# Kernel optimization log

Measured on AMD Instinct MI355X. Metric: run time of the kernel, lower is better.

## Reference

```python
import jax, jax.numpy as jnp
import numpy as np

N = 2048
HID = 1024
Z = 256
DIM = 128 + 64 * 3 + 32 * 5  # 480
FAN = 128 * 128 + 64 * 64 + 32 * 32  # total fan-in over all CG paths


def _ln(x, g, b, eps=1e-6):
    mu = jnp.mean(x, axis=-1, keepdims=True)
    var = jnp.mean((x - mu) ** 2, axis=-1, keepdims=True)
    return (x - mu) * jax.lax.rsqrt(var + eps) * g + b


def _fctp(t, w0, w1, w2):
    # FullyConnectedTensorProduct(irreps, irreps, 'HIDx0e'):
    # only l1==l2 -> 0e paths survive; CG is delta_{m1,m2}/sqrt(2l+1).
    x0 = t[:, :128]                       # 128x0e
    x1 = t[:, 128:320].reshape(-1, 64, 3)  # 64x1o
    x2 = t[:, 320:480].reshape(-1, 32, 5)  # 32x2e
    e0 = jnp.einsum('bu,bv,uvh->bh', x0, x0, w0)
    e1 = jnp.einsum('bum,bvm,uvh->bh', x1, x1, w1) / np.sqrt(3.0)
    e2 = jnp.einsum('bum,bvm,uvh->bh', x2, x2, w2) / np.sqrt(5.0)
    return (e0 + e1 + e2) / np.sqrt(float(FAN))  # component normalization


def _head(t, w0, w1, w2, W1, b1, g1, be1, W2, b2, g2, be2):
    h = _fctp(t, w0, w1, w2)
    h = jax.nn.silu(_ln(h @ W1 + b1, g1, be1))
    h = jax.nn.silu(_ln(h @ W2 + b2, g2, be2))
    return h  # [N, Z]


def setup_inputs() -> dict:
    key = jax.random.key(0)
    ks = jax.random.split(key, 6)
    return {
        'tensor_in': jax.random.normal(ks[0], (N, DIM), jnp.float32),
        'w0': jax.random.normal(ks[1], (128, 128, HID), jnp.float32),
        'w1': jax.random.normal(ks[2], (64, 64, HID), jnp.float32),
        'w2': jax.random.normal(ks[3], (32, 32, HID), jnp.float32),
        'W1': jax.random.normal(ks[4], (HID, HID), jnp.float32) / np.sqrt(HID),
        'b1': jnp.zeros((HID,), jnp.float32),
        'g1': jnp.ones((HID,), jnp.float32),
        'be1': jnp.zeros((HID,), jnp.float32),
        'W2': jax.random.normal(ks[5], (HID, Z), jnp.float32) / np.sqrt(HID),
        'b2': jnp.zeros((Z,), jnp.float32),
        'g2': jnp.ones((Z,), jnp.float32),
        'be2': jnp.zeros((Z,), jnp.float32),
    }


def reference(tensor_in, w0, w1, w2, W1, b1, g1, be1, W2, b2, g2, be2):
    f = lambda t: _head(t, w0, w1, w2, W1, b1, g1, be1, W2, b2, g2, be2)
    x, pullback = jax.vjp(f, tensor_in)
    # torch: grad(x, tensor_in, grad_outputs=ones_like(x), create_graph=True)
    y = pullback(jnp.ones_like(x))[0]
    return x, y
```

## Files before the change

kernel.cpp:

```cpp
#include <hip/hip_runtime.h>
#include <math.h>

typedef unsigned short u16;
typedef __bf16 bf16x8 __attribute__((ext_vector_type(8)));
typedef float f32x4 __attribute__((ext_vector_type(4)));

#define NPACK  11264
#define NVALID 10864
#define BASE1  8256
#define BASE2  10336

__device__ __forceinline__ u16 f2bf(float f) {
    unsigned u = __builtin_bit_cast(unsigned, f);
    u += 0x7FFFu + ((u >> 16) & 1u);
    return (u16)(u >> 16);
}
__device__ __forceinline__ float bf2f(u16 h) {
    return __builtin_bit_cast(float, ((unsigned)h) << 16);
}

#define GLOAD_LDS16(g, l)                                                     \
    __builtin_amdgcn_global_load_lds(                                         \
        (const __attribute__((address_space(1))) void*)(g),                   \
        (__attribute__((address_space(3))) void*)(l), 16, 0, 0)

__device__ __forceinline__ int pk0(int a, int b) {
    int u = min(a, b), v = max(a, b);
    return u * 128 - (u * (u - 1)) / 2 + (v - u);
}
__device__ __forceinline__ int pk1(int a, int b) {
    int u = min(a, b), v = max(a, b);
    return BASE1 + u * 64 - (u * (u - 1)) / 2 + (v - u);
}
__device__ __forceinline__ int pk2(int a, int b) {
    int u = min(a, b), v = max(a, b);
    return BASE2 + u * 32 - (u * (u - 1)) / 2 + (v - u);
}

__device__ __forceinline__ void prep_transpose(const float* __restrict__ in, int C,
                                               u16* __restrict__ out, int ldOut,
                                               int bx, int by, int tid) {
    __shared__ float tile[32][33];
    int tr0 = by * 32, tc0 = bx * 32;
    int lr = tid >> 5, lc = tid & 31;
#pragma unroll
    for (int i = 0; i < 4; i++) {
        int rr = lr + i * 8;
        tile[rr][lc] = in[(size_t)(tr0 + rr) * C + tc0 + lc];
    }
    __syncthreads();
#pragma unroll
    for (int i = 0; i < 4; i++) {
        int rr = lr + i * 8;
        out[(size_t)(tc0 + rr) * ldOut + tr0 + lc] = f2bf(tile[lc][rr]);
    }
}
__device__ __forceinline__ void prep_convert(const float* __restrict__ in,
                                             u16* __restrict__ out, int i, int n4) {
    if (i >= n4) return;
    float4 v = ((const float4*)in)[i];
    union { u16 a[4]; unsigned long long q; } o;
    o.a[0] = f2bf(v.x); o.a[1] = f2bf(v.y); o.a[2] = f2bf(v.z); o.a[3] = f2bf(v.w);
    ((unsigned long long*)out)[i] = o.q;
}

__global__ __launch_bounds__(256) void k_prep(u16* __restrict__ tab,
                                              const float* __restrict__ W1,
                                              const float* __restrict__ W2,
                                              u16* __restrict__ W1b,
                                              u16* __restrict__ W1tb,
                                              u16* __restrict__ W2b,
                                              u16* __restrict__ W2tb) {
    int bid = blockIdx.x, tid = threadIdx.x;
    if (bid < 86) {
        int j = bid * 256 + tid;
        if (j < 16384) {
            int u = j >> 7, v = j & 127;
            if (v >= u) tab[pk0(u, v)] = (u16)((u << 7) | v);
        } else if (j < 20480) {
            int k = j - 16384, u = k >> 6, v = k & 63;
            if (v >= u) tab[pk1(u, v)] = (u16)((1 << 14) | (u << 7) | v);
        } else if (j < 21504) {
            int k = j - 20480, u = k >> 5, v = k & 31;
            if (v >= u) tab[pk2(u, v)] = (u16)((2 << 14) | (u << 7) | v);
        } else if (j < 21504 + (NPACK - NVALID)) {
            tab[NVALID + (j - 21504)] = 0xFFFFu;
        }
    } else if (bid < 1110) {
        int k = bid - 86;
        prep_transpose(W1, 1024, W1tb, 1024, k & 31, k >> 5, tid);
    } else if (bid < 1366) {
        int k = bid - 1110;
        prep_transpose(W2, 256, W2tb, 1024, k & 7, k >> 3, tid);
    } else if (bid < 2390) {
        prep_convert(W1, W1b, (bid - 1366) * 256 + tid, 1024 * 1024 / 4);
    } else {
        prep_convert(W2, W2b, (bid - 2390) * 256 + tid, 1024 * 256 / 4);
    }
}

__global__ __launch_bounds__(256) void k_packw(const float* __restrict__ w0,
                                               const float* __restrict__ w1,
                                               const float* __restrict__ w2,
                                               const u16* __restrict__ tab,
                                               u16* __restrict__ Wsym,
                                               u16* __restrict__ Wt) {
    __shared__ u16 tile[32][258];
    __shared__ u16 te[32];
    int i0 = blockIdx.x * 32, h0 = blockIdx.y * 256, tid = threadIdx.x;
    if (tid < 32) te[tid] = tab[i0 + tid];
    __syncthreads();
    const float s1 = 0.57735026918962576f, s2 = 0.44721359549995794f;
    for (int il = 0; il < 32; il++) {
        unsigned e = te[il];
        float val = 0.f;
        if ((e >> 14) != 3) {
            int seg = e >> 14, u = (e >> 7) & 127, v = e & 127;
            const float* wb; int S; float sc;
            if (seg == 0)      { wb = w0; S = 128; sc = 1.f; }
            else if (seg == 1) { wb = w1; S = 64;  sc = s1; }
            else               { wb = w2; S = 32;  sc = s2; }
            val = sc * (wb[(size_t)(u * S + v) * 1024 + h0 + tid] +
                        wb[(size_t)(v * S + u) * 1024 + h0 + tid]);
        }
        u16 bv = f2bf(val);
        Wsym[(size_t)(i0 + il) * 1024 + h0 + tid] = bv;
        tile[il][tid] = bv;
    }
    __syncthreads();
    union { u16 a[32]; uint4 q[4]; } pk;
#pragma unroll
    for (int il = 0; il < 32; il++) pk.a[il] = tile[il][tid];
    uint4* dst = (uint4*)(Wt + (size_t)(h0 + tid) * NPACK + i0);
#pragma unroll
    for (int q = 0; q < 4; q++) dst[q] = pk.q[q];
}

__global__ __launch_bounds__(256) void k_features_pack(const float* __restrict__ t,
                                                       const u16* __restrict__ tab,
                                                       u16* __restrict__ P) {
    __shared__ u16 tab_s[NPACK];
    __shared__ float tr[480];
    int b = blockIdx.x, tid = threadIdx.x;
    for (int j = tid; j < NPACK / 8; j += 256)
        ((uint4*)tab_s)[j] = ((const uint4*)tab)[j];
    for (int j = tid; j < 480; j += 256) tr[j] = t[(size_t)b * 480 + j];
    __syncthreads();
    u16* row = P + (size_t)b * NPACK;
    for (int i = tid; i < NPACK; i += 256) {
        unsigned e = tab_s[i];
        float p = 0.f;
        if ((e >> 14) != 3) {
            int seg = e >> 14, u = (e >> 7) & 127, v = e & 127;
            if (seg == 0) p = tr[u] * tr[v];
            else if (seg == 1) {
                const float* x1 = tr + 128;
                p = x1[u*3]*x1[v*3] + x1[u*3+1]*x1[v*3+1] + x1[u*3+2]*x1[v*3+2];
            } else {
                const float* x2 = tr + 320;
#pragma unroll
                for (int m = 0; m < 5; m++) p += x2[u*5+m] * x2[v*5+m];
            }
            if (u == v) p *= 0.5f;
        }
        row[i] = f2bf(p);
    }
}

__global__ __launch_bounds__(256) void k_gemm2(const u16* __restrict__ A, int ldA,
                                               const u16* __restrict__ B, int ldB,
                                               int kLen, float scale,
                                               const float* __restrict__ bias,
                                               float* __restrict__ Cf,
                                               u16* __restrict__ Cb, int ldC,
                                               u16* __restrict__ Cpart, int Mtot,
                                               int swz) {
    __shared__ u16 As[2][128 * 32];
    __shared__ u16 Bs[2][128 * 32];
    const int tid = threadIdx.x;
    const int wave = tid >> 6, lane = tid & 63;
    const int wm = wave >> 1, wn = wave & 1;
    int nT, mT, z;
    if (swz == 1) {
        int L = blockIdx.x;
        z = L & 7; int r = L >> 3;
        nT = r >> 4; mT = r & 15;
    } else if (swz == 2) {
        int L = blockIdx.x;
        int c = L & 7, r = L >> 3;
        nT = (r % 11) * 8 + c; mT = r / 11; z = 0;
    } else {
        nT = blockIdx.x; mT = blockIdx.y; z = blockIdx.z;
    }
    const int m0 = mT * 128, n0 = nT * 128;
    const size_t kOff = (size_t)z * kLen;

    const int chl = (((lane & 3) ^ ((lane >> 3) & 3))) * 8;
    const u16* aG = A + (size_t)(m0 + wave * 32 + (lane >> 2)) * ldA + kOff + chl;
    const u16* bG = B + (size_t)(n0 + wave * 32 + (lane >> 2)) * ldB + kOff + chl;
    const size_t aS = (size_t)16 * ldA;
    const size_t bS = (size_t)16 * ldB;
    u16* aL0 = &As[0][(wave * 32) * 32];
    u16* aL1 = &As[0][(wave * 32 + 16) * 32];
    u16* aH0 = &As[1][(wave * 32) * 32];
    u16* aH1 = &As[1][(wave * 32 + 16) * 32];
    u16* bL0 = &Bs[0][(wave * 32) * 32];
    u16* bL1 = &Bs[0][(wave * 32 + 16) * 32];
    u16* bH0 = &Bs[1][(wave * 32) * 32];
    u16* bH1 = &Bs[1][(wave * 32 + 16) * 32];

    f32x4 acc[4][4];
#pragma unroll
    for (int i = 0; i < 4; i++)
#pragma unroll
        for (int j = 0; j < 4; j++) acc[i][j] = (f32x4){0.f, 0.f, 0.f, 0.f};

    const int ml = lane & 15, kq8 = lane >> 4;
    const int kqs = (kq8 ^ ((ml >> 1) & 3)) * 8;
    const u16* aRd0 = &As[0][(wm * 64 + ml) * 32 + kqs];
    const u16* bRd0 = &Bs[0][(wn * 64 + ml) * 32 + kqs];
    const u16* aRd1 = &As[1][(wm * 64 + ml) * 32 + kqs];
    const u16* bRd1 = &Bs[1][(wn * 64 + ml) * 32 + kqs];

    for (int k = 0; k < kLen; k += 64) {
        GLOAD_LDS16(aG, aL0);
        GLOAD_LDS16(aG + aS, aL1);
        GLOAD_LDS16(aG + 32, aH0);
        GLOAD_LDS16(aG + aS + 32, aH1);
        GLOAD_LDS16(bG, bL0);
        GLOAD_LDS16(bG + bS, bL1);
        GLOAD_LDS16(bG + 32, bH0);
        GLOAD_LDS16(bG + bS + 32, bH1);
        aG += 64; bG += 64;
        __syncthreads();
        {
            bf16x8 af[4], bfv[4];
#pragma unroll
            for (int i = 0; i < 4; i++) af[i]  = *(const bf16x8*)(aRd0 + i * 16 * 32);
#pragma unroll
            for (int j = 0; j < 4; j++) bfv[j] = *(const bf16x8*)(bRd0 + j * 16 * 32);
#pragma unroll
            for (int i = 0; i < 4; i++)
#pragma unroll
                for (int j = 0; j < 4; j++)
                    acc[i][j] = __builtin_amdgcn_mfma_f32_16x16x32_bf16(af[i], bfv[j], acc[i][j], 0, 0, 0);
        }
        {
            bf16x8 af[4], bfv[4];
#pragma unroll
            for (int i = 0; i < 4; i++) af[i]  = *(const bf16x8*)(aRd1 + i * 16 * 32);
#pragma unroll
            for (int j = 0; j < 4; j++) bfv[j] = *(const bf16x8*)(bRd1 + j * 16 * 32);
#pragma unroll
            for (int i = 0; i < 4; i++)
#pragma unroll
                for (int j = 0; j < 4; j++)
                    acc[i][j] = __builtin_amdgcn_mfma_f32_16x16x32_bf16(af[i], bfv[j], acc[i][j], 0, 0, 0);
        }
        __syncthreads();
    }

    const int q = lane >> 4, nl = lane & 15;
    if (Cpart) {
        u16* outP = Cpart + (size_t)z * Mtot * ldC;
#pragma unroll
        for (int i = 0; i < 4; i++)
#pragma unroll
            for (int j = 0; j < 4; j++)
#pragma unroll
                for (int reg = 0; reg < 4; reg++) {
                    int row = m0 + wm * 64 + i * 16 + q * 4 + reg;
                    int col = n0 + wn * 64 + j * 16 + nl;
                    outP[(size_t)row * ldC + col] = f2bf(acc[i][j][reg]);
                }
    } else {
#pragma unroll
        for (int i = 0; i < 4; i++)
#pragma unroll
            for (int j = 0; j < 4; j++)
#pragma unroll
                for (int reg = 0; reg < 4; reg++) {
                    int row = m0 + wm * 64 + i * 16 + q * 4 + reg;
                    int col = n0 + wn * 64 + j * 16 + nl;
                    float v = acc[i][j][reg] * scale + (bias ? bias[col] : 0.0f);
                    if (Cf) Cf[(size_t)row * ldC + col] = v;
                    else    Cb[(size_t)row * ldC + col] = f2bf(v);
                }
    }
}

#define VMCNT0 asm volatile("s_waitcnt vmcnt(0)" ::: "memory")
#define BARX() __builtin_amdgcn_s_barrier()

#define STG_A(p, kh, rh, kb) GLOAD_LDS16(aB + (size_t)(rh) * aH + (kb) + (kh) * 32, \
                                         &As[p][kh][((rh) * 128 + wave * 16) * 32])
#define STG_B(p, kh, rh, kb) GLOAD_LDS16(bB + (size_t)(rh) * bH + (kb) + (kh) * 32, \
                                         &Bs[p][kh][((rh) * 128 + wave * 16) * 32])
#define MMQ(fb, gb, bv) do { _Pragma("unroll") \
    for (int ff = 0; ff < 4; ff++) { _Pragma("unroll") \
        for (int gg = 0; gg < 2; gg++) { \
            acc[(fb)+ff][(gb)+gg] = __builtin_amdgcn_mfma_f32_16x16x32_bf16(a[2*ff],   bv[2*gg],   acc[(fb)+ff][(gb)+gg], 0, 0, 0); \
            acc[(fb)+ff][(gb)+gg] = __builtin_amdgcn_mfma_f32_16x16x32_bf16(a[2*ff+1], bv[2*gg+1], acc[(fb)+ff][(gb)+gg], 0, 0, 0); } } } while (0)

__global__ __launch_bounds__(512, 2) void k_gemm256(const u16* __restrict__ A, int ldA,
                                                    const u16* __restrict__ B, int ldB,
                                                    int kLen, float scale,
                                                    const float* __restrict__ bias,
                                                    u16* __restrict__ Cb, int ldC,
                                                    u16* __restrict__ Cpart, int Mtot,
                                                    int swz) {
    __shared__ __align__(16) u16 As[2][2][256 * 32];
    __shared__ __align__(16) u16 Bs[2][2][256 * 32];
    const int tid = threadIdx.x;
    const int lane = tid & 63, wave = tid >> 6;
    const int wm = wave >> 2, wn = wave & 3;
    int mT, nT, z;
    if (swz == 1) {
        z = blockIdx.x & 7; int r = blockIdx.x >> 3; nT = r & 3; mT = r >> 2;
    } else {
        int x = blockIdx.x & 7, j = blockIdx.x >> 3;
        int nti = j >> 3; mT = j & 7;
        if (nti < 5)      nT = nti * 8 + x;
        else if (x < 4)   nT = 40 + x;
        else            { nT = 40 + (x - 4); mT = (j & 7) + 4; }
        z = 0;
    }
    const int m0 = mT * 256, n0 = nT * 256;
    const size_t kOff = (size_t)z * kLen;
    const int nTi = kLen >> 6;

    const int chl = ((tid & 3) ^ ((tid >> 3) & 3)) * 8;
    const u16* aB = A + (size_t)(m0 + (tid >> 2)) * ldA + kOff + chl;
    const u16* bB = B + (size_t)(n0 + (tid >> 2)) * ldB + kOff + chl;
    const size_t aH = (size_t)128 * ldA;
    const size_t bH = (size_t)128 * ldB;

    const int ml = lane & 15, kq8 = lane >> 4;
    const int kqs = (kq8 ^ ((ml >> 1) & 3)) * 8;
    const int aro = (wm * 128 + ml) * 32 + kqs;
    const int bro = (wn * 64 + ml) * 32 + kqs;

    f32x4 acc[8][4];
#pragma unroll
    for (int f = 0; f < 8; f++)
#pragma unroll
        for (int g = 0; g < 4; g++) acc[f][g] = (f32x4){0.f, 0.f, 0.f, 0.f};
    bf16x8 a[8], b[4], b2[4];

    STG_A(0, 0, 0, 0); STG_A(0, 0, 1, 0); STG_A(0, 1, 0, 0); STG_A(0, 1, 1, 0);
    STG_B(0, 0, 0, 0); STG_B(0, 0, 1, 0); STG_B(0, 1, 0, 0); STG_B(0, 1, 1, 0);
    VMCNT0;
    BARX();

    for (int t = 0; t < nTi; t++) {
        const int p = t & 1, p1 = p ^ 1;
        const int kb1 = (t + 1) << 6;
        const bool s1 = (t + 1) < nTi;
#pragma unroll
        for (int f = 0; f < 4; f++) {
            a[2*f]   = *(const bf16x8*)&As[p][0][aro + f * 512];
            a[2*f+1] = *(const bf16x8*)&As[p][1][aro + f * 512];
        }
#pragma unroll
        for (int g = 0; g < 2; g++) {
            b[2*g]   = *(const bf16x8*)&Bs[p][0][bro + g * 512];
            b[2*g+1] = *(const bf16x8*)&Bs[p][1][bro + g * 512];
        }
        if (s1) { STG_A(p1, 0, 0, kb1); STG_A(p1, 0, 1, kb1); }
        BARX();
        __builtin_amdgcn_s_setprio(1);
        MMQ(0, 0, b);
        __builtin_amdgcn_s_setprio(0);
        BARX();
#pragma unroll
        for (int g = 0; g < 2; g++) {
            b2[2*g]   = *(const bf16x8*)&Bs[p][0][bro + (g + 2) * 512];
            b2[2*g+1] = *(const bf16x8*)&Bs[p][1][bro + (g + 2) * 512];
        }
        if (s1) { STG_A(p1, 1, 0, kb1); STG_A(p1, 1, 1, kb1); }
        BARX();
        __builtin_amdgcn_s_setprio(1);
        MMQ(0, 2, b2);
        __builtin_amdgcn_s_setprio(0);
        BARX();
#pragma unroll
        for (int f = 0; f < 4; f++) {
            a[2*f]   = *(const bf16x8*)&As[p][0][aro + (f + 4) * 512];
            a[2*f+1] = *(const bf16x8*)&As[p][1][aro + (f + 4) * 512];
        }
        if (s1) { STG_B(p1, 0, 0, kb1); STG_B(p1, 0, 1, kb1); }
        BARX();
        __builtin_amdgcn_s_setprio(1);
        MMQ(4, 0, b);
        __builtin_amdgcn_s_setprio(0);
        BARX();
        if (s1) { STG_B(p1, 1, 0, kb1); STG_B(p1, 1, 1, kb1); }
        __builtin_amdgcn_s_setprio(1);
        MMQ(4, 2, b2);
        __builtin_amdgcn_s_setprio(0);
        if (s1) VMCNT0;
        BARX();
    }

    const int q = lane >> 4, nl = lane & 15;
    if (Cpart) {
        u16* outP = Cpart + (size_t)z * Mtot * ldC;
#pragma unroll
        for (int f = 0; f < 8; f++)
#pragma unroll
            for (int g = 0; g < 4; g++)
#pragma unroll
                for (int reg = 0; reg < 4; reg++) {
                    int row = m0 + wm * 128 + f * 16 + q * 4 + reg;
                    int col = n0 + wn * 64 + g * 16 + nl;
                    outP[(size_t)row * ldC + col] = f2bf(acc[f][g][reg]);
                }
    } else {
#pragma unroll
        for (int f = 0; f < 8; f++)
#pragma unroll
            for (int g = 0; g < 4; g++)
#pragma unroll
                for (int reg = 0; reg < 4; reg++) {
                    int row = m0 + wm * 128 + f * 16 + q * 4 + reg;
                    int col = n0 + wn * 64 + g * 16 + nl;
                    float v = acc[f][g][reg] * scale + (bias ? bias[col] : 0.0f);
                    Cb[(size_t)row * ldC + col] = f2bf(v);
                }
    }
}

__global__ __launch_bounds__(256) void k_reduce(const u16* __restrict__ part, size_t stride,
                                                int SK, int total, int N, float scale,
                                                const float* __restrict__ bias,
                                                float* __restrict__ outF, u16* __restrict__ outB) {
    int i = blockIdx.x * 256 + threadIdx.x;
    if (i >= total) return;
    float s = 0.f;
    for (int z = 0; z < SK; z++) s += bf2f(part[(size_t)z * stride + i]);
    float v = s * scale + (bias ? bias[i % N] : 0.0f);
    if (outF) outF[i] = v;
    else      outB[i] = f2bf(v);
}

__device__ __forceinline__ float blockReduce(float v, float* red) {
#pragma unroll
    for (int off = 32; off > 0; off >>= 1) v += __shfl_down(v, off);
    __syncthreads();
    if ((threadIdx.x & 63) == 0) red[threadIdx.x >> 6] = v;
    __syncthreads();
    return red[0] + red[1] + red[2] + red[3];
}

__global__ __launch_bounds__(256) void k_ln_fwd(const float* __restrict__ X, int D,
    const float* __restrict__ g, const float* __restrict__ be,
    float* __restrict__ mu_out, float* __restrict__ r_out,
    u16* __restrict__ a_bf, float* __restrict__ a_f32) {
    __shared__ float red[4];
    int b = blockIdx.x, tid = threadIdx.x;
    const float* x = X + (size_t)b * D;
    int nd = D >> 8;
    float s = 0.f, s2 = 0.f;
    for (int r = 0; r < nd; r++) { float v = x[tid + (r << 8)]; s += v; s2 += v * v; }
    s = blockReduce(s, red);
    s2 = blockReduce(s2, red);
    float mu = s / D;
    float var = s2 / D - mu * mu;
    float rst = rsqrtf(var + 1e-6f);
    if (tid == 0) { mu_out[b] = mu; r_out[b] = rst; }
    for (int r = 0; r < nd; r++) {
        int i = tid + (r << 8);
        float xh = (x[i] - mu) * rst;
        float ln = xh * g[i] + be[i];
        float a = ln / (1.0f + expf(-ln));
        if (a_bf)  a_bf[(size_t)b * D + i] = f2bf(a);
        if (a_f32) a_f32[(size_t)b * D + i] = a;
    }
}

__global__ __launch_bounds__(256) void k_ln_bwd(const float* __restrict__ dup,
    const float* __restrict__ X, const float* __restrict__ mu_in, const float* __restrict__ r_in,
    const float* __restrict__ g, const float* __restrict__ be,
    u16* __restrict__ out_bf, int D) {
    __shared__ float red[4];
    int b = blockIdx.x, tid = threadIdx.x;
    const float* x = X + (size_t)b * D;
    float mu = mu_in[b], rst = r_in[b];
    int nd = D >> 8;
    float w_[4], xh_[4];
    float sw = 0.f, swx = 0.f;
    for (int r = 0; r < nd; r++) {
        int i = tid + (r << 8);
        float xh = (x[i] - mu) * rst;
        float ln = xh * g[i] + be[i];
        float sg = 1.0f / (1.0f + expf(-ln));
        float dsilu = sg * (1.0f + ln * (1.0f - sg));
        float d = dup ? dup[(size_t)b * D + i] : 1.0f;
        float w = g[i] * dsilu * d;
        w_[r] = w; xh_[r] = xh;
        sw += w; swx += w * xh;
    }
    sw = blockReduce(sw, red);
    swx = blockReduce(swx, red);
    float invD = 1.0f / D;
    for (int r = 0; r < nd; r++) {
        int i = tid + (r << 8);
        float dx = rst * (w_[r] - sw * invD - xh_[r] * swx * invD);
        out_bf[(size_t)b * D + i] = f2bf(dx);
    }
}

__global__ __launch_bounds__(256) void k_contract_p(const u16* __restrict__ Gp,
                                                    const float* __restrict__ t,
                                                    float* __restrict__ y) {
    __shared__ u16 gp_s[NPACK];
    __shared__ float xs[480];
    int b = blockIdx.x, tid = threadIdx.x;
    const uint4* gsrc = (const uint4*)(Gp + (size_t)b * NPACK);
    for (int j = tid; j < NPACK / 8; j += 256) ((uint4*)gp_s)[j] = gsrc[j];
    for (int j = tid; j < 480; j += 256) xs[j] = t[(size_t)b * 480 + j];
    __syncthreads();
    int wave = tid >> 6, lane = tid & 63;
    float* yr = y + (size_t)b * 480;
    for (int r = 0; r < 32; r++) {
        int u = wave * 32 + r;
        int v0 = lane, v1 = lane + 64;
        float s = bf2f(gp_s[pk0(u, v0)]) * xs[v0] + bf2f(gp_s[pk0(u, v1)]) * xs[v1];
#pragma unroll
        for (int off = 32; off > 0; off >>= 1) s += __shfl_down(s, off);
        if (lane == 0) yr[u] = s;
    }
    for (int r = 0; r < 16; r++) {
        int u = wave * 16 + r;
        float gv = bf2f(gp_s[pk1(u, lane)]);
        float a0 = gv * xs[128 + lane * 3 + 0];
        float a1 = gv * xs[128 + lane * 3 + 1];
        float a2 = gv * xs[128 + lane * 3 + 2];
#pragma unroll
        for (int off = 32; off > 0; off >>= 1) {
            a0 += __shfl_down(a0, off);
            a1 += __shfl_down(a1, off);
            a2 += __shfl_down(a2, off);
        }
        if (lane == 0) {
            yr[128 + u * 3 + 0] = a0;
            yr[128 + u * 3 + 1] = a1;
            yr[128 + u * 3 + 2] = a2;
        }
    }
    for (int r = 0; r < 8; r++) {
        int u = wave * 8 + r;
        bool act = lane < 32;
        float gv = act ? bf2f(gp_s[pk2(u, act ? lane : 0)]) : 0.f;
        float a[5];
#pragma unroll
        for (int m = 0; m < 5; m++)
            a[m] = act ? gv * xs[320 + lane * 5 + m] : 0.f;
#pragma unroll
        for (int off = 32; off > 0; off >>= 1)
#pragma unroll
            for (int m = 0; m < 5; m++) a[m] += __shfl_down(a[m], off);
        if (lane == 0)
#pragma unroll
            for (int m = 0; m < 5; m++) yr[320 + u * 5 + m] = a[m];
    }
}

extern "C" void kernel_launch(void* const* d_in, const int* in_sizes, int n_in,
                              void* d_out, int out_size, void* d_ws, size_t ws_size,
                              hipStream_t stream) {
    const float* t   = (const float*)d_in[0];
    const float* w0  = (const float*)d_in[1];
    const float* w1  = (const float*)d_in[2];
    const float* w2  = (const float*)d_in[3];
    const float* W1  = (const float*)d_in[4];
    const float* b1  = (const float*)d_in[5];
    const float* g1  = (const float*)d_in[6];
    const float* be1 = (const float*)d_in[7];
    const float* W2  = (const float*)d_in[8];
    const float* b2  = (const float*)d_in[9];
    const float* g2  = (const float*)d_in[10];
    const float* be2 = (const float*)d_in[11];

    float* xout = (float*)d_out;
    float* yout = xout + (size_t)2048 * 256;

    char* ws = (char*)d_ws;
    size_t off = 0;
    auto alloc = [&](size_t bytes) -> void* {
        void* p = ws + off;
        off += (bytes + 255) & ~(size_t)255;
        return p;
    };
    u16*   PG    = (u16*)alloc((size_t)2048 * NPACK * 2);
    u16*   Wsym  = (u16*)alloc((size_t)NPACK * 1024 * 2);
    u16*   Wt    = (u16*)alloc((size_t)1024 * NPACK * 2);
    u16*   uvtab = (u16*)alloc((size_t)NPACK * 2);
    u16*   W1b   = (u16*)alloc((size_t)1024 * 1024 * 2);
    u16*   W1tb  = (u16*)alloc((size_t)1024 * 1024 * 2);
    u16*   W2b   = (u16*)alloc((size_t)1024 * 256 * 2);
    u16*   W2tb  = (u16*)alloc((size_t)256 * 1024 * 2);
    u16*   h_bf  = (u16*)alloc((size_t)2048 * 1024 * 2);
    float* h1pre = (float*)alloc((size_t)2048 * 1024 * 4);
    float* mu1   = (float*)alloc(2048 * 4);
    float* r1    = (float*)alloc(2048 * 4);
    u16*   a1_bf = (u16*)alloc((size_t)2048 * 1024 * 2);
    float* h2pre = (float*)alloc((size_t)2048 * 256 * 4);
    float* mu2   = (float*)alloc(2048 * 4);
    float* r2    = (float*)alloc(2048 * 4);
    u16*   dh2b  = (u16*)alloc((size_t)2048 * 256 * 2);
    float* d_a1  = (float*)alloc((size_t)2048 * 1024 * 4);
    u16*   dh1b  = (u16*)alloc((size_t)2048 * 1024 * 2);
    u16*   de_bf = (u16*)alloc((size_t)2048 * 1024 * 2);
    u16*   Cpart = (u16*)(ws + off);
    size_t cpartBytes = (ws_size > off) ? (ws_size - off) : 0;
    (void)in_sizes; (void)n_in; (void)out_size;

    const float sF = 1.0f / sqrtf(21504.0f);

    auto gemm = [&](const u16* A, int ldA, const u16* B, int ldB, int M, int N, int K,
                    int SKwant, float scale, const float* bias,
                    float* Cf, u16* Cb, int ldC) {
        int SK = SKwant;
        size_t slice = (size_t)M * ldC * 2;
        if (SK > 1 && cpartBytes < 2 * slice) SK = 1;
        if (SK > 1 && (size_t)SK * slice > cpartBytes) SK = (int)(cpartBytes / slice);
        while (SK > 1 && !((K % SK) == 0 && ((K / SK) % 64) == 0)) SK--;
        dim3 grid(N / 128, M / 128, SK);
        if (SK > 1) {
            k_gemm2<<<grid, 256, 0, stream>>>(A, ldA, B, ldB, K / SK, 0.f, nullptr,
                                              nullptr, nullptr, ldC, Cpart, M, 0);
            int total = M * ldC;
            k_reduce<<<(total + 255) / 256, 256, 0, stream>>>(Cpart, (size_t)M * ldC, SK,
                                                              total, N, scale, bias, Cf, Cb);
        } else {
            k_gemm2<<<grid, 256, 0, stream>>>(A, ldA, B, ldB, K, scale, bias,
                                              Cf, Cb, ldC, nullptr, M, 0);
        }
    };

    k_prep<<<2646, 256, 0, stream>>>(uvtab, W1, W2, W1b, W1tb, W2b, W2tb);
    k_packw<<<dim3(NPACK / 32, 4), 256, 0, stream>>>(w0, w1, w2, uvtab, Wsym, Wt);

    k_features_pack<<<2048, 256, 0, stream>>>(t, uvtab, PG);

    k_gemm256<<<dim3(256), 512, 0, stream>>>(PG, NPACK, Wt, NPACK, NPACK / 8, 0.f, nullptr,
                                             nullptr, 1024, Cpart, 2048, 1);
    {
        int total = 2048 * 1024;
        k_reduce<<<(total + 255) / 256, 256, 0, stream>>>(Cpart, (size_t)2048 * 1024, 8,
                                                          total, 1024, sF, nullptr,
                                                          nullptr, h_bf);
    }

    gemm(h_bf, 1024, W1tb, 1024, 2048, 1024, 1024, 4, 1.0f, b1, h1pre, nullptr, 1024);
    k_ln_fwd<<<2048, 256, 0, stream>>>(h1pre, 1024, g1, be1, mu1, r1, a1_bf, nullptr);
    gemm(a1_bf, 1024, W2tb, 1024, 2048, 256, 1024, 8, 1.0f, b2, h2pre, nullptr, 256);
    k_ln_fwd<<<2048, 256, 0, stream>>>(h2pre, 256, g2, be2, mu2, r2, nullptr, xout);

    k_ln_bwd<<<2048, 256, 0, stream>>>(nullptr, h2pre, mu2, r2, g2, be2, dh2b, 256);
    gemm(dh2b, 256, W2b, 256, 2048, 1024, 256, 4, 1.0f, nullptr, d_a1, nullptr, 1024);
    k_ln_bwd<<<2048, 256, 0, stream>>>(d_a1, h1pre, mu1, r1, g1, be1, dh1b, 1024);
    gemm(dh1b, 1024, W1b, 1024, 2048, 1024, 1024, 4, sF, nullptr, nullptr, de_bf, 1024);

    u16* Gp = PG;
    k_gemm256<<<dim3(352), 512, 0, stream>>>(de_bf, 1024, Wsym, 1024, 1024, 1.0f, nullptr,
                                             Gp, NPACK, nullptr, 2048, 2);

    k_contract_p<<<2048, 256, 0, stream>>>(Gp, t, yout);
}
```

Baseline: 501.1 us.

## Replace 256x256 GEMM with 128x256-tile kernel for backward Wsym projection

Adds a dedicated GEMM kernel using 128x256 output tiles with 512 threads and two blocks per CU, launched on 704 blocks instead of 352 for the de x Wsym product. It double-buffers LDS via direct global-to-LDS loads that are interleaved between quarter-tile MFMA phases, and remaps block indices so the tail N tiles are spread across M. The aim is better CU occupancy and wave balance on the large packed-output GEMM. The cost is lower arithmetic intensity per tile and more barriers per K step.

After: 484.3 us. 1.03x faster.

```diff
diff --git a/kernel.cpp b/kernel.cpp
--- a/kernel.cpp
+++ b/kernel.cpp
@@ -428,6 +428,116 @@
                     Cb[(size_t)row * ldC + col] = f2bf(v);
                 }
     }
+}
+
+#define MMQ22(fb, gb, bv) do { _Pragma("unroll") \
+    for (int ff = 0; ff < 2; ff++) { _Pragma("unroll") \
+        for (int gg = 0; gg < 2; gg++) { \
+            acc[(fb)+ff][(gb)+gg] = __builtin_amdgcn_mfma_f32_16x16x32_bf16(a[2*ff],   bv[2*gg],   acc[(fb)+ff][(gb)+gg], 0, 0, 0); \
+            acc[(fb)+ff][(gb)+gg] = __builtin_amdgcn_mfma_f32_16x16x32_bf16(a[2*ff+1], bv[2*gg+1], acc[(fb)+ff][(gb)+gg], 0, 0, 0); } } } while (0)
+
+__global__ __launch_bounds__(512, 2) void k_gemm128n(const u16* __restrict__ A, int ldA,
+                                                     const u16* __restrict__ B, int ldB,
+                                                     int kLen, float scale,
+                                                     u16* __restrict__ Cb, int ldC) {
+    __shared__ __align__(16) u16 As[2][2][128 * 32];
+    __shared__ __align__(16) u16 Bs[2][2][256 * 32];
+    const int tid = threadIdx.x;
+    const int lane = tid & 63, wave = tid >> 6;
+    const int wm = wave >> 2, wn = wave & 3;
+    int x = blockIdx.x & 7, j = blockIdx.x >> 3;
+    int nti = j >> 4, mT = j & 15, nT;
+    if (nti < 5) nT = nti * 8 + x;
+    else { nT = 40 + (x & 3); mT = (j & 7) + 8 * (x >> 2); }
+    const int m0 = mT * 128, n0 = nT * 256;
+    const int nTi = kLen >> 6;
+
+    const int chl = ((tid & 3) ^ ((tid >> 3) & 3)) * 8;
+    const u16* aB = A + (size_t)(m0 + (tid >> 2)) * ldA + chl;
+    const u16* bB = B + (size_t)(n0 + (tid >> 2)) * ldB + chl;
+    const size_t bH = (size_t)128 * ldB;
+
+    const int ml = lane & 15, kq8 = lane >> 4;
+    const int kqs = (kq8 ^ ((ml >> 1) & 3)) * 8;
+    const int aro = (wm * 64 + ml) * 32 + kqs;
+    const int bro = (wn * 64 + ml) * 32 + kqs;
+
+    f32x4 acc[4][4];
+#pragma unroll
+    for (int f = 0; f < 4; f++)
+#pragma unroll
+        for (int g = 0; g < 4; g++) acc[f][g] = (f32x4){0.f, 0.f, 0.f, 0.f};
+    bf16x8 a[4], b[4], b2[4];
+
+#define SG_A(p, kh, kb) GLOAD_LDS16(aB + (kb) + (kh) * 32, &As[p][kh][(wave * 16) * 32])
+#define SG_B(p, kh, rh, kb) GLOAD_LDS16(bB + (size_t)(rh) * bH + (kb) + (kh) * 32, \
+                                        &Bs[p][kh][((rh) * 128 + wave * 16) * 32])
+
+    SG_A(0, 0, 0); SG_A(0, 1, 0);
+    SG_B(0, 0, 0, 0); SG_B(0, 0, 1, 0); SG_B(0, 1, 0, 0); SG_B(0, 1, 1, 0);
+    VMCNT0;
+    BARX();
+
+    for (int t = 0; t < nTi; t++) {
+        const int p = t & 1, p1 = p ^ 1;
+        const int kb1 = (t + 1) << 6;
+        const bool s1 = (t + 1) < nTi;
+#pragma unroll
+        for (int f = 0; f < 2; f++) {
+            a[2*f]   = *(const bf16x8*)&As[p][0][aro + f * 512];
+            a[2*f+1] = *(const bf16x8*)&As[p][1][aro + f * 512];
+        }
+#pragma unroll
+        for (int g = 0; g < 2; g++) {
+            b[2*g]   = *(const bf16x8*)&Bs[p][0][bro + g * 512];
+            b[2*g+1] = *(const bf16x8*)&Bs[p][1][bro + g * 512];
+        }
+        if (s1) { SG_A(p1, 0, kb1); SG_A(p1, 1, kb1); }
+        BARX();
+        __builtin_amdgcn_s_setprio(1);
+        MMQ22(0, 0, b);
+        __builtin_amdgcn_s_setprio(0);
+        BARX();
+#pragma unroll
+        for (int g = 0; g < 2; g++) {
+            b2[2*g]   = *(const bf16x8*)&Bs[p][0][bro + (g + 2) * 512];
+            b2[2*g+1] = *(const bf16x8*)&Bs[p][1][bro + (g + 2) * 512];
+        }
+        if (s1) { SG_B(p1, 0, 0, kb1); SG_B(p1, 0, 1, kb1); }
+        BARX();
+        __builtin_amdgcn_s_setprio(1);
+        MMQ22(0, 2, b2);
+        __builtin_amdgcn_s_setprio(0);
+        BARX();
+#pragma unroll
+        for (int f = 0; f < 2; f++) {
+            a[2*f]   = *(const bf16x8*)&As[p][0][aro + (f + 2) * 512];
+            a[2*f+1] = *(const bf16x8*)&As[p][1][aro + (f + 2) * 512];
+        }
+        if (s1) { SG_B(p1, 1, 0, kb1); SG_B(p1, 1, 1, kb1); }
+        BARX();
+        __builtin_amdgcn_s_setprio(1);
+        MMQ22(2, 0, b);
+        __builtin_amdgcn_s_setprio(0);
+        BARX();
+        __builtin_amdgcn_s_setprio(1);
+        MMQ22(2, 2, b2);
+        __builtin_amdgcn_s_setprio(0);
+        if (s1) VMCNT0;
+        BARX();
+    }
+
+    const int q = lane >> 4, nl = lane & 15;
+#pragma unroll
+    for (int f = 0; f < 4; f++)
+#pragma unroll
+        for (int g = 0; g < 4; g++)
+#pragma unroll
+            for (int reg = 0; reg < 4; reg++) {
+                int row = m0 + wm * 64 + f * 16 + q * 4 + reg;
+                int col = n0 + wn * 64 + g * 16 + nl;
+                Cb[(size_t)row * ldC + col] = f2bf(acc[f][g][reg] * scale);
+            }
 }
 
 __global__ __launch_bounds__(256) void k_reduce(const u16* __restrict__ part, size_t stride,
@@ -664,8 +774,8 @@
     gemm(dh1b, 1024, W1b, 1024, 2048, 1024, 1024, 4, sF, nullptr, nullptr, de_bf, 1024);
 
     u16* Gp = PG;
-    k_gemm256<<<dim3(352), 512, 0, stream>>>(de_bf, 1024, Wsym, 1024, 1024, 1.0f, nullptr,
-                                             Gp, NPACK, nullptr, 2048, 2);
+    k_gemm128n<<<dim3(704), 512, 0, stream>>>(de_bf, 1024, Wsym, 1024, 1024, 1.0f,
+                                              Gp, NPACK);
 
     k_contract_p<<<2048, 256, 0, stream>>>(Gp, t, yout);
 }
```
